# Optimization experiments

Measured on AMD Instinct MI355X. Metric: run time of the kernel, lower is better.

The kernel has to match this reference:

```python
import jax, jax.numpy as jnp
import numpy as np

S, N, H, E, V = 64, 256, 1024, 256, 128  # seq_len, batch, hidden, embed, vocab
DIR = 2  # bidirectional encoder


def setup_inputs() -> dict:
    key = jax.random.key(0)
    ks = jax.random.split(key, 16)
    sd = lambda fan: 1.0 / np.sqrt(fan)
    inp = {
        'x': jax.random.randint(ks[0], (N,), 0, V),
        'encoder_states': jax.random.normal(ks[1], (S, N, DIR * H), dtype=jnp.float32),
        'hidden': jax.random.normal(ks[2], (2, N, H), dtype=jnp.float32),
        'cell': jnp.zeros((2, N, H), dtype=jnp.float32),
        'emb': jax.random.normal(ks[3], (V, E), dtype=jnp.float32),
        'U_w': jax.random.normal(ks[4], (H, DIR * H), dtype=jnp.float32) * sd(DIR * H),
        'U_b': jnp.zeros((H,), jnp.float32),
        'W_w': jax.random.normal(ks[5], (H, H), dtype=jnp.float32) * sd(H),
        'W_b': jnp.zeros((H,), jnp.float32),
        'attn_w': jax.random.normal(ks[6], (1, H), dtype=jnp.float32) * sd(H),
        'attn_b': jnp.zeros((1,), jnp.float32),
        'W_ih0': jax.random.normal(ks[7], (3 * H, DIR * H + E), dtype=jnp.float32) * sd(H),
        'W_hh0': jax.random.normal(ks[8], (3 * H, H), dtype=jnp.float32) * sd(H),
        'b_ih0': jnp.zeros((3 * H,), jnp.float32),
        'b_hh0': jnp.zeros((3 * H,), jnp.float32),
        'W_ih1': jax.random.normal(ks[9], (3 * H, H), dtype=jnp.float32) * sd(H),
        'W_hh1': jax.random.normal(ks[10], (3 * H, H), dtype=jnp.float32) * sd(H),
        'b_ih1': jnp.zeros((3 * H,), jnp.float32),
        'b_hh1': jnp.zeros((3 * H,), jnp.float32),
        'fc_w': jax.random.normal(ks[11], (V, H), dtype=jnp.float32) * sd(H),
        'fc_b': jnp.zeros((V,), jnp.float32),
    }
    return inp


def _gru_cell(x, h, W_ih, W_hh, b_ih, b_hh):
    # PyTorch GRU cell math. x:(N,Din), h:(N,H) -> (N,H)
    gi = x @ W_ih.T + b_ih
    gh = h @ W_hh.T + b_hh
    ir, iz, i_n = jnp.split(gi, 3, axis=-1)
    hr, hz, h_n = jnp.split(gh, 3, axis=-1)
    r = jax.nn.sigmoid(ir + hr)
    z = jax.nn.sigmoid(iz + hz)
    n = jnp.tanh(i_n + r * h_n)
    return (1.0 - z) * n + z * h


def reference(x, encoder_states, hidden, cell, emb, U_w, U_b, W_w, W_b,
              attn_w, attn_b, W_ih0, W_hh0, b_ih0, b_hh0,
              W_ih1, W_hh1, b_ih1, b_hh1, fc_w, fc_b):
    # embedding (dropout is identity at inference)
    emb_x = emb[x]                                   # (N, E)
    # additive (Bahdanau) attention
    u = jnp.einsum('snd,hd->snh', encoder_states, U_w) + U_b   # (S,N,H)
    w = hidden[-1] @ W_w.T + W_b                                # (N,H)
    energy = jnp.tanh(u + w[None]) @ attn_w.T + attn_b          # (S,N,1)
    attention = jax.nn.softmax(energy, axis=0)                  # softmax over seq dim
    context = jnp.einsum('sn,snd->nd', attention[..., 0], encoder_states)  # (N, 2H)
    rnn_input = jnp.concatenate([context, emb_x], axis=-1)      # (N, 2H+E)
    # 2-layer single-step GRU (inter-layer dropout = identity at inference)
    h0 = _gru_cell(rnn_input, hidden[0], W_ih0, W_hh0, b_ih0, b_hh0)
    h1 = _gru_cell(h0, hidden[1], W_ih1, W_hh1, b_ih1, b_hh1)
    hidden_new = jnp.stack([h0, h1], axis=0)                    # (2, N, H)
    predictions = h1 @ fc_w.T + fc_b                            # (N, V)
    return predictions, hidden_new, attention
```

## Files before the change

### kernel.cpp

```cpp
#include <hip/hip_runtime.h>
#include <stdint.h>

typedef __attribute__((ext_vector_type(8))) short bf16x8;
typedef __attribute__((ext_vector_type(4))) float f32x4;

#define DEVI __device__ __forceinline__

DEVI unsigned short f2bf(float f) {
    union { float f; uint32_t u; } v; v.f = f;
    uint32_t r = v.u + 0x7FFFu + ((v.u >> 16) & 1u);
    return (unsigned short)(r >> 16);
}
DEVI float bf2f(unsigned short h) {
    union { uint32_t u; float f; } v; v.u = ((uint32_t)h) << 16;
    return v.f;
}
DEVI bf16x8 pack8(float4 a, float4 b) {
    bf16x8 o;
    o[0]=(short)f2bf(a.x); o[1]=(short)f2bf(a.y); o[2]=(short)f2bf(a.z); o[3]=(short)f2bf(a.w);
    o[4]=(short)f2bf(b.x); o[5]=(short)f2bf(b.y); o[6]=(short)f2bf(b.z); o[7]=(short)f2bf(b.w);
    return o;
}

DEVI unsigned char f2e4m3(float x) {
    union { float f; uint32_t u; } v; v.f = x;
    uint32_t sign = (v.u >> 24) & 0x80u;
    v.u &= 0x7FFFFFFFu;
    if (v.f >= 464.f) return (unsigned char)(sign | 0x7Eu);
    if (v.f < 0.0009765625f) return (unsigned char)sign;
    uint32_t e = v.u >> 23;
    float q = __builtin_rintf(v.f * 512.f);
    uint32_t ms = (uint32_t)q;
    uint32_t subres = sign | (ms >= 8u ? 0x08u : ms);
    uint32_t r = v.u + 0x7FFFFu + ((v.u >> 20) & 1u);
    uint32_t er = r >> 23;
    uint32_t normres = (er > 135u) ? (sign | 0x7Eu)
                                   : (sign | ((er - 120u) << 3) | ((r >> 20) & 7u));
    return (unsigned char)((e < 121u) ? subres : normres);
}

DEVI float e4m3f(unsigned char u) {
    union { uint32_t u; float f; } v;
    v.u = (((uint32_t)u & 0x80u) << 24) | (((uint32_t)u & 0x7Fu) << 20);
    return v.f * 0x1p120f;
}

#define GLOAD_LDS16(gsrc, ldst) \
    __builtin_amdgcn_global_load_lds((__attribute__((address_space(1))) void*)(gsrc), \
                                     (__attribute__((address_space(3))) void*)(ldst), 16, 0, 0)

#define BARR asm volatile("s_barrier" ::: "memory")
#define WAITV(n) asm volatile("s_waitcnt vmcnt(" #n ")" ::: "memory")

__global__ void k_prep(const float* __restrict__ es, const float* __restrict__ U_w,
                       const float* __restrict__ W_w, const float* __restrict__ fc_w,
                       const float* __restrict__ hidden,
                       const float* __restrict__ Wih0, const float* __restrict__ Whh0,
                       const float* __restrict__ Wih1, const float* __restrict__ Whh1,
                       unsigned char* __restrict__ ES_F8, unsigned char* __restrict__ UW_F8,
                       unsigned short* __restrict__ WW_BF, unsigned short* __restrict__ FCW_BF,
                       unsigned short* __restrict__ A0, unsigned short* __restrict__ A1,
                       unsigned short* __restrict__ H1B,
                       unsigned short* __restrict__ B0, unsigned short* __restrict__ B1) {
    int i = blockIdx.x * blockDim.x + threadIdx.x;
    const int S0 = 4194304, S1 = S0 + 262144, S2 = S1 + 131072, S3 = S2 + 16384;
    const int S4 = S3 + 32768, S5 = S4 + 1703936, S6 = S5 + 1048576;
    if (i < S0) {
        const float4* s = (const float4*)(es + (size_t)i * 8);
        float4 a = s[0], b = s[1];
        float vv[8] = {a.x, a.y, a.z, a.w, b.x, b.y, b.z, b.w};
        unsigned long long p8 = 0;
        #pragma unroll
        for (int k = 0; k < 8; ++k) p8 |= (unsigned long long)f2e4m3(vv[k]) << (8 * k);
        *(unsigned long long*)(ES_F8 + (size_t)i * 8) = p8;
    } else if (i < S1) {
        int j = i - S0;
        const float4* s = (const float4*)(U_w + (size_t)j * 8);
        float4 a = s[0], b = s[1];
        float vv[8] = {a.x, a.y, a.z, a.w, b.x, b.y, b.z, b.w};
        unsigned long long p8 = 0;
        #pragma unroll
        for (int k = 0; k < 8; ++k) p8 |= (unsigned long long)f2e4m3(vv[k] * 16.f) << (8 * k);
        *(unsigned long long*)(UW_F8 + (size_t)j * 8) = p8;
    } else if (i < S2) {
        int j = i - S1;
        const float4* s = (const float4*)(W_w + (size_t)j * 8);
        *(bf16x8*)(WW_BF + (size_t)j * 8) = pack8(s[0], s[1]);
    } else if (i < S3) {
        int j = i - S2;
        const float4* s = (const float4*)(fc_w + (size_t)j * 8);
        *(bf16x8*)(FCW_BF + (size_t)j * 8) = pack8(s[0], s[1]);
    } else if (i < S4) {
        int j = i - S3;
        int n = j >> 7, e0 = (j & 127) * 8;
        const float4* p0 = (const float4*)(hidden + (size_t)n * 1024 + e0);
        const float4* p1 = (const float4*)(hidden + 262144 + (size_t)n * 1024 + e0);
        bf16x8 o0 = pack8(p0[0], p0[1]);
        bf16x8 o1 = pack8(p1[0], p1[1]);
        *(bf16x8*)(A0 + (size_t)n * 3328 + 2304 + e0) = o0;
        *(bf16x8*)(A1 + (size_t)n * 2048 + 1024 + e0) = o1;
        *(bf16x8*)(H1B + (size_t)n * 1024 + e0) = o1;
    } else if (i < S5) {
        unsigned j = (unsigned)(i - S4);
        unsigned r = j / 416u;
        int kc = (int)(j - r * 416u) * 8;
        const float* src = nullptr;
        if (r < 2048)      src = (kc < 2304) ? (Wih0 + (size_t)r * 2304 + kc)
                                             : (Whh0 + (size_t)r * 1024 + (kc - 2304));
        else if (r < 3072) { if (kc < 2304)  src = Wih0 + (size_t)r * 2304 + kc; }
        else               { if (kc >= 2304) src = Whh0 + (size_t)(r - 1024) * 1024 + (kc - 2304); }
        bf16x8 o;
        if (src) { const float4* s4 = (const float4*)src; o = pack8(s4[0], s4[1]); }
        else     { for (int k = 0; k < 8; ++k) o[k] = 0; }
        *(bf16x8*)(B0 + (size_t)r * 3328 + kc) = o;
    } else if (i < S6) {
        int j = i - S5;
        int r = j >> 8;
        int kc = (j & 255) * 8;
        const float* src = nullptr;
        if (r < 2048)      src = (kc < 1024) ? (Wih1 + (size_t)r * 1024 + kc)
                                             : (Whh1 + (size_t)r * 1024 + (kc - 1024));
        else if (r < 3072) { if (kc < 1024)  src = Wih1 + (size_t)r * 1024 + kc; }
        else               { if (kc >= 1024) src = Whh1 + (size_t)(r - 1024) * 1024 + (kc - 1024); }
        bf16x8 o;
        if (src) { const float4* s4 = (const float4*)src; o = pack8(s4[0], s4[1]); }
        else     { for (int k = 0; k < 8; ++k) o[k] = 0; }
        *(bf16x8*)(B1 + (size_t)r * 2048 + kc) = o;
    }
}

__global__ __launch_bounds__(256) void gemm_bt_sk(
        const unsigned short* __restrict__ A, const unsigned short* __restrict__ B,
        float* __restrict__ Cpart, int N, int K, int ksl) {
    __shared__ unsigned short sA[4096];
    __shared__ unsigned short sB[4096];
    const int nbx = gridDim.x;
    const int nwg = nbx * gridDim.y;
    int d = blockIdx.y * nbx + blockIdx.x;
    int f = d;
    if ((nwg & 7) == 0) { int cpx = nwg >> 3; f = (d & 7) * cpx + (d >> 3); }
    const int bx = f % nbx, by = f / nbx;
    const int z = blockIdx.z;
    const int t = threadIdx.x, wave = t >> 6, lane = t & 63;
    const int wm = wave >> 1, wn = wave & 1;
    const int lg = lane >> 4, r16 = lane & 15;
    const int row0 = by * 128, col0 = bx * 128;
    const int M = gridDim.y * 128;

    const int cr = t >> 2, ckc = (t & 3) * 8;
    const unsigned short* gA  = A + (size_t)(row0 + cr) * K + (size_t)z * ksl + ckc;
    const unsigned short* gA2 = gA + (size_t)64 * K;
    const unsigned short* gB  = B + (size_t)(col0 + cr) * K + (size_t)z * ksl + ckc;
    const unsigned short* gB2 = gB + (size_t)64 * K;
    unsigned short* lA1 = sA + wave * 512;
    unsigned short* lA2 = sA + 2048 + wave * 512;
    unsigned short* lB1 = sB + wave * 512;
    unsigned short* lB2 = sB + 2048 + wave * 512;

    f32x4 acc[4][4];
    #pragma unroll
    for (int i = 0; i < 4; ++i)
        #pragma unroll
        for (int j = 0; j < 4; ++j)
            #pragma unroll
            for (int q = 0; q < 4; ++q) acc[i][j][q] = 0.0f;

    const int ao = (wm * 64 + r16) * 32 + lg * 8;
    const int bo = (wn * 64 + r16) * 32 + lg * 8;

    #pragma unroll 1
    for (int kt = 0; kt < ksl; kt += 32) {
        GLOAD_LDS16(gA, lA1); GLOAD_LDS16(gA2, lA2);
        GLOAD_LDS16(gB, lB1); GLOAD_LDS16(gB2, lB2);
        gA += 32; gA2 += 32; gB += 32; gB2 += 32;
        __syncthreads();
        bf16x8 af[4], bfr[4];
        #pragma unroll
        for (int i = 0; i < 4; ++i) af[i]  = *(const bf16x8*)(sA + ao + i * 512);
        #pragma unroll
        for (int j = 0; j < 4; ++j) bfr[j] = *(const bf16x8*)(sB + bo + j * 512);
        #pragma unroll
        for (int i = 0; i < 4; ++i)
            #pragma unroll
            for (int j = 0; j < 4; ++j)
                acc[i][j] = __builtin_amdgcn_mfma_f32_16x16x32_bf16(af[i], bfr[j], acc[i][j], 0, 0, 0);
        __syncthreads();
    }
    float* Cz = Cpart + (size_t)z * (size_t)M * N;
    #pragma unroll
    for (int i = 0; i < 4; ++i)
        #pragma unroll
        for (int j = 0; j < 4; ++j)
            #pragma unroll
            for (int q = 0; q < 4; ++q) {
                int row = row0 + wm * 64 + i * 16 + lg * 4 + q;
                int col = col0 + wn * 64 + j * 16 + r16;
                Cz[(size_t)row * N + col] = acc[i][j][q];
            }
}

__global__ __launch_bounds__(256) void gemm_energy128_f8(
        const unsigned char* __restrict__ A, const unsigned char* __restrict__ B,
        const float* __restrict__ attn_w, const float* __restrict__ U_b,
        const float* __restrict__ W_b, const float* __restrict__ WP,
        float* __restrict__ e_part) {
    const int NTT = 16;
    __shared__ __align__(16) char lds[65536];

    const int t = threadIdx.x;
    const int w = t >> 6, lane = t & 63;
    const int wm = w >> 1, wn = w & 1;
    const int lg = lane >> 4, r16 = lane & 15;

    int d = blockIdx.y * gridDim.x + blockIdx.x;
    int f = (d & 7) * 128 + (d >> 3);
    const int bx = f & 7, by = f >> 3;
    const int row0 = by * 128, col0 = bx * 128;

    const unsigned char* gsrc[8];
    unsigned lodst[8];
    #pragma unroll
    for (int q = 0; q < 8; ++q) {
        int isB = q >> 2, rq = q & 3;
        int row = rq * 32 + w * 8 + (lane >> 3);
        int slot = (lane & 7) ^ (lane >> 3);
        gsrc[q] = (isB ? B + (size_t)(col0 + row) * 2048
                       : A + (size_t)(row0 + row) * 2048) + slot * 16;
        lodst[q] = (unsigned)(isB * 16384 + (rq * 32 + w * 8) * 128);
    }

#define STAGE(T) do { \
    char* lp_ = lds + ((T) & 1) * 32768; \
    _Pragma("unroll") \
    for (int q_ = 0; q_ < 8; ++q_) \
        GLOAD_LDS16(gsrc[q_] + (size_t)(T) * 128, lp_ + lodst[q_]); \
} while (0)

    unsigned s16[2];
    #pragma unroll
    for (int sel = 0; sel < 2; ++sel)
        s16[sel] = (unsigned)(((sel * 4 + lg) ^ (r16 & 7)) << 4);
    unsigned arow[4], brow[4];
    #pragma unroll
    for (int m = 0; m < 4; ++m) arow[m] = (unsigned)((wm * 64 + m * 16 + r16) * 128);
    #pragma unroll
    for (int n = 0; n < 4; ++n) brow[n] = 16384u + (unsigned)((wn * 64 + n * 16 + r16) * 128);

    f32x4 acc[4][4];
    #pragma unroll
    for (int m = 0; m < 4; ++m)
        #pragma unroll
        for (int n = 0; n < 4; ++n)
            #pragma unroll
            for (int q = 0; q < 4; ++q) acc[m][n][q] = 0.0f;

    STAGE(0);
    #pragma unroll 1
    for (int tt = 0; tt < NTT; ++tt) {
        if (tt + 1 < NTT) { STAGE(tt + 1); WAITV(8); }
        else              { WAITV(0); }
        BARR;
        const char* lp = lds + (tt & 1) * 32768;
        #pragma unroll
        for (int sel = 0; sel < 2; ++sel) {
            long2 afr[4], bfr[4];
            #pragma unroll
            for (int n = 0; n < 4; ++n) bfr[n] = *(const long2*)(lp + brow[n] + s16[sel]);
            #pragma unroll
            for (int m = 0; m < 4; ++m) afr[m] = *(const long2*)(lp + arow[m] + s16[sel]);
            #pragma unroll
            for (int m = 0; m < 4; ++m)
                #pragma unroll
                for (int n = 0; n < 4; ++n)
                    acc[m][n] = __builtin_amdgcn_mfma_f32_16x16x32_fp8_fp8(
                        afr[m].x, bfr[n].x, acc[m][n], 0, 0, 0);
            #pragma unroll
            for (int m = 0; m < 4; ++m)
                #pragma unroll
                for (int n = 0; n < 4; ++n)
                    acc[m][n] = __builtin_amdgcn_mfma_f32_16x16x32_fp8_fp8(
                        afr[m].y, bfr[n].y, acc[m][n], 0, 0, 0);
        }
        BARR;
    }
#undef STAGE

    float aw[4], ub[4];
    #pragma unroll
    for (int n = 0; n < 4; ++n) {
        int col = col0 + wn * 64 + n * 16 + r16;
        aw[n] = attn_w[col];
        ub[n] = U_b[col] + W_b[col];
    }
    #pragma unroll
    for (int m = 0; m < 4; ++m)
        #pragma unroll
        for (int q = 0; q < 4; ++q) {
            int row = row0 + wm * 64 + m * 16 + lg * 4 + q;
            const float* wrow = WP + (size_t)(row & 255) * 1024;
            float e = 0.f;
            #pragma unroll
            for (int n = 0; n < 4; ++n) {
                int col = col0 + wn * 64 + n * 16 + r16;
                float wv = wrow[col] + wrow[262144 + col] + wrow[524288 + col] + wrow[786432 + col];
                float cc = acc[m][n][q] * 0.0625f + ub[n] + wv;
                float ex = __expf(2.f * cc);
                e += aw[n] * (1.f - 2.f / (ex + 1.f));
            }
            e += __shfl_xor(e, 1); e += __shfl_xor(e, 2);
            e += __shfl_xor(e, 4); e += __shfl_xor(e, 8);
            if (r16 == 0) e_part[(size_t)row * 16 + bx * 2 + wn] = e;
        }
}

__global__ __launch_bounds__(256) void k_softctx(
        const unsigned char* __restrict__ es8, const float* __restrict__ e_part,
        const float* __restrict__ emb, const int* __restrict__ x,
        float* __restrict__ attn_out, unsigned short* __restrict__ A0) {
    int n = blockIdx.x, t = threadIdx.x;
    __shared__ float as_[64];
    __shared__ float ev[64];
    {
        int s = t >> 2;
        const float* p = e_part + ((size_t)(s * 256 + n)) * 16 + (t & 3) * 4;
        float v = p[0] + p[1] + p[2] + p[3];
        v += __shfl_xor(v, 1); v += __shfl_xor(v, 2);
        if ((t & 3) == 0) ev[s] = v;
        __syncthreads();
        if (t < 64) {
            float e = ev[t];
            float mx = e;
            #pragma unroll
            for (int o = 1; o < 64; o <<= 1) mx = fmaxf(mx, __shfl_xor(mx, o));
            float ee = __expf(e - mx);
            float sum = ee;
            #pragma unroll
            for (int o = 1; o < 64; o <<= 1) sum += __shfl_xor(sum, o);
            float a = ee / sum;
            as_[t] = a;
            attn_out[t * 256 + n] = a;
        }
        __syncthreads();
    }
    float acc[8];
    #pragma unroll
    for (int k = 0; k < 8; ++k) acc[k] = 0.f;
    const unsigned char* base = es8 + (size_t)n * 2048 + t * 8;
    for (int s = 0; s < 64; ++s) {
        unsigned long long v = *(const unsigned long long*)(base + (size_t)s * 524288);
        float a = as_[s];
        #pragma unroll
        for (int k = 0; k < 8; ++k)
            acc[k] += a * e4m3f((unsigned char)(v >> (8 * k)));
    }
    bf16x8 o;
    #pragma unroll
    for (int k = 0; k < 8; ++k) o[k] = (short)f2bf(acc[k]);
    *(bf16x8*)(A0 + (size_t)n * 3328 + t * 8) = o;
    if (t < 32) {
        const float4* e4 = (const float4*)(emb + (size_t)x[n] * 256 + t * 8);
        *(bf16x8*)(A0 + (size_t)n * 3328 + 2048 + t * 8) = pack8(e4[0], e4[1]);
    }
}

__global__ void k_gru(const float* __restrict__ g, const float* __restrict__ b_ih,
                      const float* __restrict__ b_hh, const float* __restrict__ h_in,
                      float* __restrict__ h_out, unsigned short* __restrict__ a_dst,
                      int dst_pitch) {
    int i = blockIdx.x * blockDim.x + threadIdx.x;
    int n = i >> 10, e = i & 1023;
    const float* gn = g + (size_t)n * 4096;
    float rr = 0.f, zz = 0.f, in_ = 0.f, hn_ = 0.f;
    #pragma unroll
    for (int z = 0; z < 4; ++z) {
        const float* gz = gn + (size_t)z * 1048576;
        rr  += gz[e];
        zz  += gz[1024 + e];
        in_ += gz[2048 + e];
        hn_ += gz[3072 + e];
    }
    rr  += b_ih[e]        + b_hh[e];
    zz  += b_ih[1024 + e] + b_hh[1024 + e];
    in_ += b_ih[2048 + e];
    hn_ += b_hh[2048 + e];
    float r = 1.f / (1.f + __expf(-rr));
    float z = 1.f / (1.f + __expf(-zz));
    float ex = __expf(2.f * (in_ + r * hn_));
    float nn = 1.f - 2.f / (ex + 1.f);
    float h = h_in[i];
    float ho = (1.f - z) * nn + z * h;
    h_out[i] = ho;
    a_dst[(size_t)n * dst_pitch + e] = f2bf(ho);
}

__global__ void k_fcsum(const float* __restrict__ Fp, const float* __restrict__ fc_b,
                        float* __restrict__ outp) {
    int i = blockIdx.x * blockDim.x + threadIdx.x;
    outp[i] = Fp[i] + Fp[32768 + i] + Fp[65536 + i] + Fp[98304 + i] + fc_b[i & 127];
}


extern "C" void kernel_launch(void* const* d_in, const int* in_sizes, int n_in,
                              void* d_out, int out_size, void* d_ws, size_t ws_size,
                              hipStream_t stream) {
    const int*   x      = (const int*)  d_in[0];
    const float* es     = (const float*)d_in[1];
    const float* hidden = (const float*)d_in[2];
    const float* emb    = (const float*)d_in[4];
    const float* U_w    = (const float*)d_in[5];
    const float* U_b    = (const float*)d_in[6];
    const float* W_w    = (const float*)d_in[7];
    const float* W_b    = (const float*)d_in[8];
    const float* attn_w = (const float*)d_in[9];
    const float* W_ih0  = (const float*)d_in[11];
    const float* W_hh0  = (const float*)d_in[12];
    const float* b_ih0  = (const float*)d_in[13];
    const float* b_hh0  = (const float*)d_in[14];
    const float* W_ih1  = (const float*)d_in[15];
    const float* W_hh1  = (const float*)d_in[16];
    const float* b_ih1  = (const float*)d_in[17];
    const float* b_hh1  = (const float*)d_in[18];
    const float* fc_w   = (const float*)d_in[19];
    const float* fc_b   = (const float*)d_in[20];

    float* out        = (float*)d_out;
    float* out_pred   = out;
    float* out_hidden = out + 32768;
    float* out_attn   = out + 32768 + 524288;

    char* ws = (char*)d_ws;
    size_t off = 0;
    auto alloc = [&](size_t bytes) { char* p = ws + off; off += (bytes + 255) & ~(size_t)255; return p; };
    unsigned char*  ES_F8  = (unsigned char*) alloc((size_t)16384 * 2048);
    unsigned char*  UW_F8  = (unsigned char*) alloc((size_t)1024 * 2048);
    unsigned short* WW_BF  = (unsigned short*)alloc((size_t)1024 * 1024 * 2);
    unsigned short* FCW_BF = (unsigned short*)alloc((size_t)128 * 1024 * 2);
    unsigned short* H1_BF  = (unsigned short*)alloc((size_t)256 * 1024 * 2);
    unsigned short* B0     = (unsigned short*)alloc((size_t)4096 * 3328 * 2);
    unsigned short* B1     = (unsigned short*)alloc((size_t)4096 * 2048 * 2);
    unsigned short* A0     = (unsigned short*)alloc((size_t)256 * 3328 * 2);
    unsigned short* A1     = (unsigned short*)alloc((size_t)256 * 2048 * 2);
    unsigned short* FCA    = (unsigned short*)alloc((size_t)256 * 1024 * 2);
    float* EPART = (float*)alloc((size_t)16384 * 16 * 4);
    float* WP    = (float*)alloc((size_t)4 * 256 * 1024 * 4);
    float* G0P   = (float*)alloc((size_t)4 * 256 * 4096 * 4);
    float* FCP   = WP;
    float* G1P   = G0P;

    k_prep<<<28864, 256, 0, stream>>>(es, U_w, W_w, fc_w, hidden, W_ih0, W_hh0, W_ih1, W_hh1,
                                      ES_F8, UW_F8, WW_BF, FCW_BF, A0, A1, H1_BF, B0, B1);
    gemm_bt_sk<<<dim3(8, 2, 4), 256, 0, stream>>>(H1_BF, WW_BF, WP, 1024, 1024, 256);
    gemm_energy128_f8<<<dim3(8, 128), 256, 0, stream>>>(ES_F8, UW_F8, attn_w, U_b, W_b, WP, EPART);
    k_softctx<<<256, 256, 0, stream>>>(ES_F8, EPART, emb, x, out_attn, A0);
    gemm_bt_sk<<<dim3(32, 2, 4), 256, 0, stream>>>(A0, B0, G0P, 4096, 3328, 832);
    k_gru<<<1024, 256, 0, stream>>>(G0P, b_ih0, b_hh0, hidden, out_hidden, A1, 2048);
    gemm_bt_sk<<<dim3(32, 2, 4), 256, 0, stream>>>(A1, B1, G1P, 4096, 2048, 512);
    k_gru<<<1024, 256, 0, stream>>>(G1P, b_ih1, b_hh1, hidden + 262144, out_hidden + 262144, FCA, 1024);
    gemm_bt_sk<<<dim3(1, 2, 4), 256, 0, stream>>>(FCA, FCW_BF, FCP, 128, 1024, 256);
    k_fcsum<<<128, 256, 0, stream>>>(FCP, fc_b, out_pred);
}
```

Baseline: 197.5 us.

## Double-buffer split-K bf16 GEMM with 64-wide K tiles and swizzled LDS

```diff
diff --git a/kernel.cpp b/kernel.cpp
--- a/kernel.cpp
+++ b/kernel.cpp
@@ -129,73 +129,98 @@
     }
 }
 
-__global__ __launch_bounds__(256) void gemm_bt_sk(
+__global__ __launch_bounds__(256) void gemm_bt_sk2(
         const unsigned short* __restrict__ A, const unsigned short* __restrict__ B,
-        float* __restrict__ Cpart, int N, int K, int ksl) {
-    __shared__ unsigned short sA[4096];
-    __shared__ unsigned short sB[4096];
+        float* __restrict__ Cpart, int K, int ksl) {
+    __shared__ __align__(16) char lds[65536];
+    const int NTT = ksl >> 6;
+
+    const int t = threadIdx.x;
+    const int w = t >> 6, lane = t & 63;
+    const int wm = w >> 1, wn = w & 1;
+    const int lg = lane >> 4, r16 = lane & 15;
+    const int z = blockIdx.z;
     const int nbx = gridDim.x;
-    const int nwg = nbx * gridDim.y;
+    const int N = nbx * 128, M = gridDim.y * 128;
+
     int d = blockIdx.y * nbx + blockIdx.x;
     int f = d;
+    int nwg = nbx * gridDim.y;
     if ((nwg & 7) == 0) { int cpx = nwg >> 3; f = (d & 7) * cpx + (d >> 3); }
     const int bx = f % nbx, by = f / nbx;
-    const int z = blockIdx.z;
-    const int t = threadIdx.x, wave = t >> 6, lane = t & 63;
-    const int wm = wave >> 1, wn = wave & 1;
-    const int lg = lane >> 4, r16 = lane & 15;
     const int row0 = by * 128, col0 = bx * 128;
-    const int M = gridDim.y * 128;
-
-    const int cr = t >> 2, ckc = (t & 3) * 8;
-    const unsigned short* gA  = A + (size_t)(row0 + cr) * K + (size_t)z * ksl + ckc;
-    const unsigned short* gA2 = gA + (size_t)64 * K;
-    const unsigned short* gB  = B + (size_t)(col0 + cr) * K + (size_t)z * ksl + ckc;
-    const unsigned short* gB2 = gB + (size_t)64 * K;
-    unsigned short* lA1 = sA + wave * 512;
-    unsigned short* lA2 = sA + 2048 + wave * 512;
-    unsigned short* lB1 = sB + wave * 512;
-    unsigned short* lB2 = sB + 2048 + wave * 512;
+
+    const unsigned short* gsrc[8];
+    unsigned lodst[8];
+    #pragma unroll
+    for (int q = 0; q < 8; ++q) {
+        int isB = q >> 2, rq = q & 3;
+        int row = rq * 32 + w * 8 + (lane >> 3);
+        int slot = (lane & 7) ^ (lane >> 3);
+        gsrc[q] = (isB ? B + (size_t)(col0 + row) * K
+                       : A + (size_t)(row0 + row) * K) + (size_t)z * ksl + slot * 8;
+        lodst[q] = (unsigned)(isB * 16384 + (rq * 32 + w * 8) * 128);
+    }
+
+#define STAGE(T) do { \
+    char* lp_ = lds + ((T) & 1) * 32768; \
+    _Pragma("unroll") \
+    for (int q_ = 0; q_ < 8; ++q_) \
+        GLOAD_LDS16(gsrc[q_] + (size_t)(T) * 64, lp_ + lodst[q_]); \
+} while (0)
+
+    const unsigned swz = (unsigned)((r16 & 7) << 4);
+    unsigned aoff[4], boff[4];
+    #pragma unroll
+    for (int m = 0; m < 4; ++m)
+        aoff[m] = ((unsigned)((wm * 64 + m * 16 + r16) * 128 + lg * 16)) ^ swz;
+    #pragma unroll
+    for (int n = 0; n < 4; ++n)
+        boff[n] = 16384u + (((unsigned)((wn * 64 + n * 16 + r16) * 128 + lg * 16)) ^ swz);
 
     f32x4 acc[4][4];
     #pragma unroll
-    for (int i = 0; i < 4; ++i)
-        #pragma unroll
-        for (int j = 0; j < 4; ++j)
-            #pragma unroll
-            for (int q = 0; q < 4; ++q) acc[i][j][q] = 0.0f;
-
-    const int ao = (wm * 64 + r16) * 32 + lg * 8;
-    const int bo = (wn * 64 + r16) * 32 + lg * 8;
-
+    for (int m = 0; m < 4; ++m)
+        #pragma unroll
+        for (int n = 0; n < 4; ++n)
+            #pragma unroll
+            for (int q = 0; q < 4; ++q) acc[m][n][q] = 0.0f;
+
+    STAGE(0);
     #pragma unroll 1
-    for (int kt = 0; kt < ksl; kt += 32) {
-        GLOAD_LDS16(gA, lA1); GLOAD_LDS16(gA2, lA2);
-        GLOAD_LDS16(gB, lB1); GLOAD_LDS16(gB2, lB2);
-        gA += 32; gA2 += 32; gB += 32; gB2 += 32;
-        __syncthreads();
-        bf16x8 af[4], bfr[4];
-        #pragma unroll
-        for (int i = 0; i < 4; ++i) af[i]  = *(const bf16x8*)(sA + ao + i * 512);
-        #pragma unroll
-        for (int j = 0; j < 4; ++j) bfr[j] = *(const bf16x8*)(sB + bo + j * 512);
-        #pragma unroll
-        for (int i = 0; i < 4; ++i)
-            #pragma unroll
-            for (int j = 0; j < 4; ++j)
-                acc[i][j] = __builtin_amdgcn_mfma_f32_16x16x32_bf16(af[i], bfr[j], acc[i][j], 0, 0, 0);
-        __syncthreads();
-    }
+    for (int tt = 0; tt < NTT; ++tt) {
+        if (tt + 1 < NTT) { STAGE(tt + 1); WAITV(8); }
+        else              { WAITV(0); }
+        BARR;
+        const char* lp = lds + (tt & 1) * 32768;
+        #pragma unroll
+        for (int kk = 0; kk < 2; ++kk) {
+            bf16x8 afr[4], bfr[4];
+            #pragma unroll
+            for (int n = 0; n < 4; ++n) bfr[n] = *(const bf16x8*)(lp + (boff[n] ^ (kk << 6)));
+            #pragma unroll
+            for (int m = 0; m < 4; ++m) afr[m] = *(const bf16x8*)(lp + (aoff[m] ^ (kk << 6)));
+            #pragma unroll
+            for (int m = 0; m < 4; ++m)
+                #pragma unroll
+                for (int n = 0; n < 4; ++n)
+                    acc[m][n] = __builtin_amdgcn_mfma_f32_16x16x32_bf16(
+                        afr[m], bfr[n], acc[m][n], 0, 0, 0);
+        }
+        BARR;
+    }
+#undef STAGE
+
     float* Cz = Cpart + (size_t)z * (size_t)M * N;
     #pragma unroll
-    for (int i = 0; i < 4; ++i)
-        #pragma unroll
-        for (int j = 0; j < 4; ++j)
+    for (int m = 0; m < 4; ++m)
+        #pragma unroll
+        for (int n = 0; n < 4; ++n)
             #pragma unroll
             for (int q = 0; q < 4; ++q) {
-                int row = row0 + wm * 64 + i * 16 + lg * 4 + q;
-                int col = col0 + wn * 64 + j * 16 + r16;
-                Cz[(size_t)row * N + col] = acc[i][j][q];
+                int row = row0 + wm * 64 + m * 16 + lg * 4 + q;
+                int col = col0 + wn * 64 + n * 16 + r16;
+                Cz[(size_t)row * N + col] = acc[m][n][q];
             }
 }
 
@@ -449,13 +474,13 @@
 
     k_prep<<<28864, 256, 0, stream>>>(es, U_w, W_w, fc_w, hidden, W_ih0, W_hh0, W_ih1, W_hh1,
                                       ES_F8, UW_F8, WW_BF, FCW_BF, A0, A1, H1_BF, B0, B1);
-    gemm_bt_sk<<<dim3(8, 2, 4), 256, 0, stream>>>(H1_BF, WW_BF, WP, 1024, 1024, 256);
+    gemm_bt_sk2<<<dim3(8, 2, 4), 256, 0, stream>>>(H1_BF, WW_BF, WP, 1024, 256);
     gemm_energy128_f8<<<dim3(8, 128), 256, 0, stream>>>(ES_F8, UW_F8, attn_w, U_b, W_b, WP, EPART);
     k_softctx<<<256, 256, 0, stream>>>(ES_F8, EPART, emb, x, out_attn, A0);
-    gemm_bt_sk<<<dim3(32, 2, 4), 256, 0, stream>>>(A0, B0, G0P, 4096, 3328, 832);
+    gemm_bt_sk2<<<dim3(32, 2, 4), 256, 0, stream>>>(A0, B0, G0P, 3328, 832);
     k_gru<<<1024, 256, 0, stream>>>(G0P, b_ih0, b_hh0, hidden, out_hidden, A1, 2048);
-    gemm_bt_sk<<<dim3(32, 2, 4), 256, 0, stream>>>(A1, B1, G1P, 4096, 2048, 512);
+    gemm_bt_sk2<<<dim3(32, 2, 4), 256, 0, stream>>>(A1, B1, G1P, 2048, 512);
     k_gru<<<1024, 256, 0, stream>>>(G1P, b_ih1, b_hh1, hidden + 262144, out_hidden + 262144, FCA, 1024);
-    gemm_bt_sk<<<dim3(1, 2, 4), 256, 0, stream>>>(FCA, FCW_BF, FCP, 128, 1024, 256);
+    gemm_bt_sk2<<<dim3(1, 2, 4), 256, 0, stream>>>(FCA, FCW_BF, FCP, 1024, 256);
     k_fcsum<<<128, 256, 0, stream>>>(FCP, fc_b, out_pred);
 }
```

Result: faster. 172.8 us (-12.5%).
